# Kernel optimization log

Measured on AMD Instinct MI355X. Metric: run time of the kernel, lower is better.

Reference implementation:

```python
import jax, jax.numpy as jnp
import numpy as np
from jax import lax

EPS = 1e-5
C = 232          # inp == oup
BF = C // 2      # branch_features
GROUPS = 2


def bn(x, g, b, m, v):
    # inference batchnorm over channel axis 1 of NCHW
    scale = g / jnp.sqrt(v + EPS)
    return x * scale[None, :, None, None] + (b - m * scale)[None, :, None, None]


def prelu(x, a):
    return jnp.where(x >= 0, x, a.reshape(()) * x)


def conv1x1(x, w):
    # x: [B,C,H,W], w: [O,C]
    return jnp.einsum('bchw,oc->bohw', x, w)


def dwconv3x3(x, w):
    # depthwise 3x3, stride 1, pad 1; w: [C,1,3,3]
    return lax.conv_general_dilated(
        x, w, window_strides=(1, 1), padding=((1, 1), (1, 1)),
        feature_group_count=x.shape[1],
        dimension_numbers=('NCHW', 'OIHW', 'NCHW'))


def setup_inputs() -> dict:
    key = jax.random.key(0)
    ks = jax.random.split(key, 12)
    B, H, W = 64, 56, 56
    inp = {
        'x': jax.random.normal(ks[0], (B, C, H, W), jnp.float32),
        'w2': jax.random.normal(ks[1], (BF, BF), jnp.float32) * 0.1,
        'bn1_g': jax.random.uniform(ks[2], (BF,), jnp.float32, 0.5, 1.5),
        'bn1_b': jax.random.normal(ks[3], (BF,), jnp.float32) * 0.1,
        'bn1_m': jax.random.normal(ks[4], (BF,), jnp.float32) * 0.1,
        'bn1_v': jax.random.uniform(ks[5], (BF,), jnp.float32, 0.5, 1.5),
        'alpha1': jnp.full((1,), 0.25, jnp.float32),
        'wdw': jax.random.normal(ks[6], (BF, 1, 3, 3), jnp.float32) * 0.1,
        'bn2_g': jax.random.uniform(ks[7], (BF,), jnp.float32, 0.5, 1.5),
        'bn2_b': jax.random.normal(ks[8], (BF,), jnp.float32) * 0.1,
        'bn2_m': jax.random.normal(ks[9], (BF,), jnp.float32) * 0.1,
        'bn2_v': jax.random.uniform(ks[10], (BF,), jnp.float32, 0.5, 1.5),
        'w3': jax.random.normal(ks[11], (BF, BF), jnp.float32) * 0.1,
        'bn3_g': jax.random.uniform(jax.random.fold_in(key, 101), (BF,), jnp.float32, 0.5, 1.5),
        'bn3_b': jax.random.normal(jax.random.fold_in(key, 102), (BF,)) * 0.1,
        'bn3_m': jax.random.normal(jax.random.fold_in(key, 103), (BF,)) * 0.1,
        'bn3_v': jax.random.uniform(jax.random.fold_in(key, 104), (BF,), jnp.float32, 0.5, 1.5),
        'alpha2': jnp.full((1,), 0.25, jnp.float32),
    }
    return inp


def reference(x, w2, bn1_g, bn1_b, bn1_m, bn1_v, alpha1, wdw,
              bn2_g, bn2_b, bn2_m, bn2_v, w3, bn3_g, bn3_b, bn3_m, bn3_v, alpha2):
    # stride == 1 path: split channels in half
    x1, x2 = x[:, :BF], x[:, BF:]
    # branch2: 1x1 conv -> BN -> PReLU -> dw3x3 -> BN -> 1x1 conv -> BN -> PReLU
    h = prelu(bn(conv1x1(x2, w2), bn1_g, bn1_b, bn1_m, bn1_v), alpha1)
    h = bn(dwconv3x3(h, wdw), bn2_g, bn2_b, bn2_m, bn2_v)
    h = prelu(bn(conv1x1(h, w3), bn3_g, bn3_b, bn3_m, bn3_v), alpha2)
    out = jnp.concatenate([x1, h], axis=1)
    # channel shuffle (groups=2): out channel k reads input channel (k%2)*cpg + k//2
    cpg = C // GROUPS
    idx = (jnp.arange(C) % GROUPS) * cpg + jnp.arange(C) // GROUPS
    return out[:, idx]
```

## Files before the change

### kernel.cpp

```cpp
#include <hip/hip_runtime.h>
#include <hip/hip_bf16.h>


#define BATCH 64
#define CTOT  232
#define BFC   116
#define HW    3136
#define WD    56
#define CH2   120
#define EPSV  1e-5f

typedef unsigned short u16;
typedef __attribute__((ext_vector_type(8))) short short8;
typedef __attribute__((ext_vector_type(4))) float float4v;

#define WS_W2P   0
#define WS_W3P   32768
#define WS_WDWT  65536
#define WS_B1P   69888
#define WS_B3P   70400

__device__ __forceinline__ u16 f2bf(float f) {
    union { float f; unsigned u; } v; v.f = f;
    unsigned r = v.u + 0x7FFF + ((v.u >> 16) & 1);
    return (u16)(r >> 16);
}
__device__ __forceinline__ float bf2f(u16 u) {
    union { unsigned u; float f; } v; v.u = ((unsigned)u) << 16;
    return v.f;
}

__global__ __launch_bounds__(256) void prep(
    const float* __restrict__ w2, const float* __restrict__ g1, const float* __restrict__ b1,
    const float* __restrict__ m1, const float* __restrict__ v1,
    const float* __restrict__ wdw,
    const float* __restrict__ g2, const float* __restrict__ b2,
    const float* __restrict__ m2, const float* __restrict__ v2,
    const float* __restrict__ w3, const float* __restrict__ g3, const float* __restrict__ b3,
    const float* __restrict__ m3, const float* __restrict__ v3,
    char* __restrict__ ws) {
    u16* w2p = (u16*)(ws + WS_W2P);
    u16* w3p = (u16*)(ws + WS_W3P);
    float* wdwt = (float*)(ws + WS_WDWT);
    float* b1p = (float*)(ws + WS_B1P);
    float* b3p = (float*)(ws + WS_B3P);
    int tid = threadIdx.x;
    int bx = blockIdx.x;
    if (bx < 8) {
        int o = bx * 16 + (tid >> 4);
        int cs = (tid & 15) * 8;
        float sc = (o < BFC) ? g1[o] * rsqrtf(v1[o] + EPSV) : 0.f;
        short8 v;
        for (int j = 0; j < 8; j++) {
            int c = cs + j;
            float val = (o < BFC && c < BFC) ? sc * w2[o * BFC + c] : 0.f;
            ((u16*)&v)[j] = f2bf(val);
        }
        *(short8*)&w2p[o * 128 + cs] = v;
    } else if (bx < 16) {
        int o = (bx - 8) * 16 + (tid >> 4);
        int cs = (tid & 15) * 8;
        float sc = (o < BFC) ? g3[o] * rsqrtf(v3[o] + EPSV) : 0.f;
        short8 v;
        for (int j = 0; j < 8; j++) {
            int c = cs + j;
            float val = 0.f;
            if (o < BFC && c < BFC) {
                float sc2 = g2[c] * rsqrtf(v2[c] + EPSV);
                val = sc * sc2 * w3[o * BFC + c];
            }
            ((u16*)&v)[j] = f2bf(val);
        }
        *(short8*)&w3p[o * 128 + cs] = v;
    } else {
        if (tid < CH2)
            for (int tap = 0; tap < 9; tap++)
                wdwt[tap * CH2 + tid] = (tid < BFC) ? wdw[tid * 9 + tap] : 0.f;
        if (tid < 128) {
            float b1v = 0.f, b3v = 0.f;
            if (tid < BFC) {
                float sc1 = g1[tid] * rsqrtf(v1[tid] + EPSV);
                b1v = b1[tid] - m1[tid] * sc1;
                float sc3 = g3[tid] * rsqrtf(v3[tid] + EPSV);
                float s = 0.f;
                for (int c = 0; c < BFC; c++) {
                    float sc2 = g2[c] * rsqrtf(v2[c] + EPSV);
                    float sh2 = b2[c] - m2[c] * sc2;
                    s += w3[tid * BFC + c] * sh2;
                }
                b3v = (b3[tid] - m3[tid] * sc3) + sc3 * s;
            }
            b1p[tid] = b1v;
            b3p[tid] = b3v;
        }
    }
}

__device__ __forceinline__ void dw_compute(const u16* xs, const float* __restrict__ wdwt,
                                           int u, short8 hrow[4]) {
    int oct = u % 15;
    int pq = u / 15;
    int rr = pq / 14;
    int col0 = (pq % 14) * 4;
    float acc[4][8];
    #pragma unroll
    for (int i = 0; i < 4; i++)
        #pragma unroll
        for (int j = 0; j < 8; j++) acc[i][j] = 0.f;
    #pragma unroll
    for (int dy = 0; dy < 3; dy++) {
        int lr = rr + dy;
        float f[6][8];
        #pragma unroll
        for (int k = 0; k < 6; k++) {
            int ci = col0 - 1 + k;
            if (ci >= 0 && ci < WD) {
                short8 v = *(const short8*)&xs[(lr * WD + ci) * CH2 + oct * 8];
                #pragma unroll
                for (int j = 0; j < 8; j++) f[k][j] = bf2f(((const u16*)&v)[j]);
            } else {
                #pragma unroll
                for (int j = 0; j < 8; j++) f[k][j] = 0.f;
            }
        }
        #pragma unroll
        for (int dx = 0; dx < 3; dx++) {
            const float* wt = &wdwt[(dy * 3 + dx) * CH2 + oct * 8];
            float4v w0 = *(const float4v*)&wt[0];
            float4v w1 = *(const float4v*)&wt[4];
            float w8[8] = {w0[0], w0[1], w0[2], w0[3], w1[0], w1[1], w1[2], w1[3]};
            #pragma unroll
            for (int i = 0; i < 4; i++)
                #pragma unroll
                for (int j = 0; j < 8; j++)
                    acc[i][j] += f[i + dx][j] * w8[j];
        }
    }
    #pragma unroll
    for (int i = 0; i < 4; i++) {
        short8 ov;
        #pragma unroll
        for (int j = 0; j < 8; j++) ((u16*)&ov)[j] = f2bf(acc[i][j]);
        hrow[i] = ov;
    }
}

__global__ __launch_bounds__(256, 3) void k1(const float* __restrict__ x,
        const float* __restrict__ al1, const float* __restrict__ al2,
        const char* __restrict__ ws, float* __restrict__ out) {
    __shared__ u16 xs[224 * CH2];
    const u16* w2p = (const u16*)(ws + WS_W2P);
    const u16* w3p = (const u16*)(ws + WS_W3P);
    const float* wdwt = (const float*)(ws + WS_WDWT);
    const float* b1p = (const float*)(ws + WS_B1P);
    const float* b3p = (const float*)(ws + WS_B3P);

    int tid = threadIdx.x;
    int lane = tid & 63;
    int w = tid >> 6;
    int l15 = lane & 15, kq = lane >> 4;

    int L = blockIdx.x;
    int sw = (L & 7) * 224 + (L >> 3);
    int b = sw / 28;
    int s = sw - b * 28;
    int r0 = s * 2;
    int p_in0 = r0 * WD - WD;
    int p_out0 = r0 * WD;

    const float* x2 = x + ((size_t)b * CTOT + BFC) * HW;
    float a1 = al1[0];
    float a2 = al2[0];
    short8 z8 = {0, 0, 0, 0, 0, 0, 0, 0};

    #pragma unroll 4
    for (int it = 0; it < 14; it++) {
        int u = it * 256 + tid;
        int c2 = (u >> 3) & 63;
        if (c2 < 60) {
            int q = (u >> 9) * 8 + (u & 7);
            int p = p_in0 + q * 4;
            unsigned pr[4] = {0u, 0u, 0u, 0u};
            if (c2 < 58 && p >= 0 && p < HW) {
                int c = 2 * c2;
                float4v va = *(const float4v*)&x2[(size_t)c * HW + p];
                float4v vb = *(const float4v*)&x2[(size_t)(c + 1) * HW + p];
                #pragma unroll
                for (int j = 0; j < 4; j++)
                    pr[j] = (unsigned)f2bf(va[j]) | ((unsigned)f2bf(vb[j]) << 16);
            }
            int px = q * 4;
            #pragma unroll
            for (int j = 0; j < 4; j++)
                *(unsigned*)&xs[(px + j) * CH2 + 2 * c2] = pr[j];
        }
    }
    __syncthreads();

    {
        short8 bfr[2][4];
        float biasv[2];
        for (int ni = 0; ni < 2; ni++) {
            int o = (2 * w + ni) * 16 + l15;
            #pragma unroll
            for (int kt = 0; kt < 4; kt++)
                bfr[ni][kt] = *(const short8*)&w2p[o * 128 + kt * 32 + kq * 8];
            biasv[ni] = b1p[o];
        }
        for (int mt = 0; mt < 14; mt++) {
            int pl = mt * 16 + l15;
            const u16* arow = &xs[pl * CH2];
            short8 afr[4];
            #pragma unroll
            for (int kt = 0; kt < 4; kt++) {
                short8 av = z8;
                if (!(kt == 3 && kq == 3)) av = *(const short8*)&arow[kt * 32 + kq * 8];
                afr[kt] = av;
            }
            float4v acc[2];
            #pragma unroll
            for (int ni = 0; ni < 2; ni++) {
                acc[ni] = (float4v){0.f, 0.f, 0.f, 0.f};
                #pragma unroll
                for (int kt = 0; kt < 4; kt++)
                    acc[ni] = __builtin_amdgcn_mfma_f32_16x16x32_bf16(afr[kt], bfr[ni][kt], acc[ni], 0, 0, 0);
            }
            __syncthreads();
            #pragma unroll
            for (int ni = 0; ni < 2; ni++) {
                int o = (2 * w + ni) * 16 + l15;
                if (o < CH2) {
                    int plb = mt * 16 + kq * 4;
                    #pragma unroll
                    for (int r = 0; r < 4; r++) {
                        int pl2 = plb + r;
                        int pim = p_in0 + pl2;
                        float y = acc[ni][r] + biasv[ni];
                        y = y >= 0.f ? y : a1 * y;
                        xs[pl2 * CH2 + o] = (pim >= 0 && pim < HW) ? f2bf(y) : (u16)0;
                    }
                }
            }
        }
    }
    __syncthreads();

    short8 hA[4], hB[4];
    int uA = tid, uB = tid + 256;
    bool hasB = uB < 420;
    dw_compute(xs, wdwt, uA, hA);
    if (hasB) dw_compute(xs, wdwt, uB, hB);
    __syncthreads();
    {
        int oct = uA % 15, pq = uA / 15;
        int pl = (pq / 14) * WD + (pq % 14) * 4;
        #pragma unroll
        for (int i = 0; i < 4; i++)
            *(short8*)&xs[(pl + i) * CH2 + oct * 8] = hA[i];
    }
    if (hasB) {
        int oct = uB % 15, pq = uB / 15;
        int pl = (pq / 14) * WD + (pq % 14) * 4;
        #pragma unroll
        for (int i = 0; i < 4; i++)
            *(short8*)&xs[(pl + i) * CH2 + oct * 8] = hB[i];
    }
    __syncthreads();

    {
        int mh = w >> 1, nh = w & 1;
        short8 cfr[4][4];
        float bias3v[4];
        for (int ni = 0; ni < 4; ni++) {
            int o = (nh * 4 + ni) * 16 + l15;
            #pragma unroll
            for (int kt = 0; kt < 4; kt++)
                cfr[ni][kt] = *(const short8*)&w3p[o * 128 + kt * 32 + kq * 8];
            bias3v[ni] = b3p[o];
        }
        #pragma unroll
        for (int mi = 0; mi < 4; mi++) {
            int mt = mh * 4 + mi;
            if (mt < 7) {
                int pl = mt * 16 + l15;
                const u16* arow = &xs[pl * CH2];
                short8 afr[4];
                #pragma unroll
                for (int kt = 0; kt < 4; kt++) {
                    short8 av = z8;
                    if (!(kt == 3 && kq == 3)) av = *(const short8*)&arow[kt * 32 + kq * 8];
                    afr[kt] = av;
                }
                for (int ni = 0; ni < 4; ni++) {
                    float4v acc = {0.f, 0.f, 0.f, 0.f};
                    #pragma unroll
                    for (int kt = 0; kt < 4; kt++)
                        acc = __builtin_amdgcn_mfma_f32_16x16x32_bf16(afr[kt], cfr[ni][kt], acc, 0, 0, 0);
                    int o = (nh * 4 + ni) * 16 + l15;
                    int pq = mt * 16 + kq * 4;
                    if (o < BFC) {
                        float4v ov;
                        #pragma unroll
                        for (int r = 0; r < 4; r++) {
                            float y = acc[r] + bias3v[ni];
                            ov[r] = y >= 0.f ? y : a2 * y;
                        }
                        *(float4v*)&out[((size_t)b * CTOT + 2 * o + 1) * HW + p_out0 + pq] = ov;
                    }
                }
            }
        }
    }

    {
        const float* x1 = x + (size_t)b * CTOT * HW;
        for (int u = tid; u < BFC * 28; u += 256) {
            int c = u / 28, i = u % 28;
            float4v v = *(const float4v*)&x1[(size_t)c * HW + p_out0 + i * 4];
            *(float4v*)&out[((size_t)b * CTOT + 2 * c) * HW + p_out0 + i * 4] = v;
        }
    }
}

extern "C" void kernel_launch(void* const* d_in, const int* in_sizes, int n_in,
                              void* d_out, int out_size, void* d_ws, size_t ws_size,
                              hipStream_t stream) {
    const float* x   = (const float*)d_in[0];
    const float* w2  = (const float*)d_in[1];
    const float* g1  = (const float*)d_in[2];
    const float* b1  = (const float*)d_in[3];
    const float* m1  = (const float*)d_in[4];
    const float* v1  = (const float*)d_in[5];
    const float* al1 = (const float*)d_in[6];
    const float* wdw = (const float*)d_in[7];
    const float* g2  = (const float*)d_in[8];
    const float* b2  = (const float*)d_in[9];
    const float* m2  = (const float*)d_in[10];
    const float* v2  = (const float*)d_in[11];
    const float* w3  = (const float*)d_in[12];
    const float* g3  = (const float*)d_in[13];
    const float* b3  = (const float*)d_in[14];
    const float* m3  = (const float*)d_in[15];
    const float* v3  = (const float*)d_in[16];
    const float* al2 = (const float*)d_in[17];
    float* out = (float*)d_out;
    char* ws = (char*)d_ws;

    hipLaunchKernelGGL(prep, dim3(17), dim3(256), 0, stream,
                       w2, g1, b1, m1, v1, wdw, g2, b2, m2, v2, w3, g3, b3, m3, v3, ws);
    hipLaunchKernelGGL(k1, dim3(28 * BATCH), dim3(256), 0, stream, x, al1, al2, ws, out);
}
```

Before: 575.7 us.

## Partition work by pixel rows per wave to remove block barriers in first GEMM

Each wave now loads and converts its own band of pixel rows and runs the first 1x1 conv over its own M tiles for all output channels. This removes the block-wide barrier after the load and the per-tile barrier inside the first GEMM. The second 1x1 conv is likewise split by M tile per wave over all N, and the x1 passthrough copy moves earlier so its traffic overlaps the depthwise stage. In exchange, weights are reloaded from global or cache per M tile instead of being held in registers, and wave 3 gets less work than the others.

Result: slower. 671.8 us (+16.7%).

```diff
diff --git a/kernel.cpp b/kernel.cpp
--- a/kernel.cpp
+++ b/kernel.cpp
@@ -173,74 +173,89 @@
     float a2 = al2[0];
     short8 z8 = {0, 0, 0, 0, 0, 0, 0, 0};
 
-    #pragma unroll 4
-    for (int it = 0; it < 14; it++) {
-        int u = it * 256 + tid;
-        int c2 = (u >> 3) & 63;
-        if (c2 < 60) {
-            int q = (u >> 9) * 8 + (u & 7);
-            int p = p_in0 + q * 4;
-            unsigned pr[4] = {0u, 0u, 0u, 0u};
-            if (c2 < 58 && p >= 0 && p < HW) {
-                int c = 2 * c2;
-                float4v va = *(const float4v*)&x2[(size_t)c * HW + p];
-                float4v vb = *(const float4v*)&x2[(size_t)(c + 1) * HW + p];
-                #pragma unroll
-                for (int j = 0; j < 4; j++)
-                    pr[j] = (unsigned)f2bf(va[j]) | ((unsigned)f2bf(vb[j]) << 16);
-            }
-            int px = q * 4;
-            #pragma unroll
-            for (int j = 0; j < 4; j++)
-                *(unsigned*)&xs[(px + j) * CH2 + 2 * c2] = pr[j];
-        }
-    }
-    __syncthreads();
+    int mt0 = w * 4;
+    int mtn = (w == 3) ? 2 : 4;
+    int row0 = w * 64;
+    int nrows = (w == 3) ? 32 : 64;
 
     {
-        short8 bfr[2][4];
-        float biasv[2];
-        for (int ni = 0; ni < 2; ni++) {
-            int o = (2 * w + ni) * 16 + l15;
-            #pragma unroll
-            for (int kt = 0; kt < 4; kt++)
-                bfr[ni][kt] = *(const short8*)&w2p[o * 128 + kt * 32 + kq * 8];
-            biasv[ni] = b1p[o];
-        }
-        for (int mt = 0; mt < 14; mt++) {
-            int pl = mt * 16 + l15;
-            const u16* arow = &xs[pl * CH2];
-            short8 afr[4];
-            #pragma unroll
-            for (int kt = 0; kt < 4; kt++) {
-                short8 av = z8;
-                if (!(kt == 3 && kq == 3)) av = *(const short8*)&arow[kt * 32 + kq * 8];
-                afr[kt] = av;
-            }
-            float4v acc[2];
+        int q = lane & 7;
+        int c2l = lane >> 3;
+        for (int rc = 0; rc < nrows; rc += 32) {
+            #pragma unroll
+            for (int c2b = 0; c2b < 64; c2b += 8) {
+                int c2 = c2b + c2l;
+                if (c2 < 60) {
+                    int row = row0 + rc + q * 4;
+                    int p = p_in0 + row;
+                    unsigned pr[4] = {0u, 0u, 0u, 0u};
+                    if (c2 < 58 && p >= 0 && p < HW) {
+                        int c = 2 * c2;
+                        float4v va = *(const float4v*)&x2[(size_t)c * HW + p];
+                        float4v vb = *(const float4v*)&x2[(size_t)(c + 1) * HW + p];
+                        #pragma unroll
+                        for (int j = 0; j < 4; j++)
+                            pr[j] = (unsigned)f2bf(va[j]) | ((unsigned)f2bf(vb[j]) << 16);
+                    }
+                    #pragma unroll
+                    for (int j = 0; j < 4; j++)
+                        *(unsigned*)&xs[(row + j) * CH2 + 2 * c2] = pr[j];
+                }
+            }
+        }
+    }
+
+    for (int mi = 0; mi < mtn; mi++) {
+        int mt = mt0 + mi;
+        int pl = mt * 16 + l15;
+        const u16* arow = &xs[pl * CH2];
+        short8 afr[4];
+        #pragma unroll
+        for (int kt = 0; kt < 4; kt++) {
+            short8 av = z8;
+            if (!(kt == 3 && kq == 3)) av = *(const short8*)&arow[kt * 32 + kq * 8];
+            afr[kt] = av;
+        }
+        #pragma unroll
+        for (int nh = 0; nh < 4; nh++) {
+            short8 bfr[2][4];
+            float biasv[2];
             #pragma unroll
             for (int ni = 0; ni < 2; ni++) {
-                acc[ni] = (float4v){0.f, 0.f, 0.f, 0.f};
+                int o = nh * 32 + ni * 16 + l15;
                 #pragma unroll
                 for (int kt = 0; kt < 4; kt++)
-                    acc[ni] = __builtin_amdgcn_mfma_f32_16x16x32_bf16(afr[kt], bfr[ni][kt], acc[ni], 0, 0, 0);
-            }
-            __syncthreads();
+                    bfr[ni][kt] = *(const short8*)&w2p[o * 128 + kt * 32 + kq * 8];
+                biasv[ni] = b1p[o];
+            }
             #pragma unroll
             for (int ni = 0; ni < 2; ni++) {
-                int o = (2 * w + ni) * 16 + l15;
+                float4v acc = {0.f, 0.f, 0.f, 0.f};
+                #pragma unroll
+                for (int kt = 0; kt < 4; kt++)
+                    acc = __builtin_amdgcn_mfma_f32_16x16x32_bf16(afr[kt], bfr[ni][kt], acc, 0, 0, 0);
+                int o = nh * 32 + ni * 16 + l15;
                 if (o < CH2) {
                     int plb = mt * 16 + kq * 4;
                     #pragma unroll
                     for (int r = 0; r < 4; r++) {
                         int pl2 = plb + r;
                         int pim = p_in0 + pl2;
-                        float y = acc[ni][r] + biasv[ni];
+                        float y = acc[r] + biasv[ni];
                         y = y >= 0.f ? y : a1 * y;
                         xs[pl2 * CH2 + o] = (pim >= 0 && pim < HW) ? f2bf(y) : (u16)0;
                     }
                 }
             }
+        }
+    }
+
+    {
+        const float* x1 = x + (size_t)b * CTOT * HW;
+        for (int u = tid; u < BFC * 28; u += 256) {
+            int c = u / 28, i = u % 28;
+            float4v v = *(const float4v*)&x1[(size_t)c * HW + p_out0 + i * 4];
+            *(float4v*)&out[((size_t)b * CTOT + 2 * c) * HW + p_out0 + i * 4] = v;
         }
     }
     __syncthreads();
@@ -268,35 +283,38 @@
     __syncthreads();
 
     {
-        int mh = w >> 1, nh = w & 1;
-        short8 cfr[4][4];
-        float bias3v[4];
-        for (int ni = 0; ni < 4; ni++) {
-            int o = (nh * 4 + ni) * 16 + l15;
-            #pragma unroll
-            for (int kt = 0; kt < 4; kt++)
-                cfr[ni][kt] = *(const short8*)&w3p[o * 128 + kt * 32 + kq * 8];
-            bias3v[ni] = b3p[o];
-        }
-        #pragma unroll
-        for (int mi = 0; mi < 4; mi++) {
-            int mt = mh * 4 + mi;
-            if (mt < 7) {
-                int pl = mt * 16 + l15;
-                const u16* arow = &xs[pl * CH2];
-                short8 afr[4];
-                #pragma unroll
-                for (int kt = 0; kt < 4; kt++) {
-                    short8 av = z8;
-                    if (!(kt == 3 && kq == 3)) av = *(const short8*)&arow[kt * 32 + kq * 8];
-                    afr[kt] = av;
-                }
-                for (int ni = 0; ni < 4; ni++) {
+        int ct0 = w * 2;
+        int ctn = (w == 3) ? 1 : 2;
+        for (int mi = 0; mi < ctn; mi++) {
+            int mt = ct0 + mi;
+            int pl = mt * 16 + l15;
+            const u16* arow = &xs[pl * CH2];
+            short8 afr[4];
+            #pragma unroll
+            for (int kt = 0; kt < 4; kt++) {
+                short8 av = z8;
+                if (!(kt == 3 && kq == 3)) av = *(const short8*)&arow[kt * 32 + kq * 8];
+                afr[kt] = av;
+            }
+            #pragma unroll
+            for (int nh = 0; nh < 4; nh++) {
+                short8 cfr[2][4];
+                float bias3v[2];
+                #pragma unroll
+                for (int ni = 0; ni < 2; ni++) {
+                    int o = nh * 32 + ni * 16 + l15;
+                    #pragma unroll
+                    for (int kt = 0; kt < 4; kt++)
+                        cfr[ni][kt] = *(const short8*)&w3p[o * 128 + kt * 32 + kq * 8];
+                    bias3v[ni] = b3p[o];
+                }
+                #pragma unroll
+                for (int ni = 0; ni < 2; ni++) {
                     float4v acc = {0.f, 0.f, 0.f, 0.f};
                     #pragma unroll
                     for (int kt = 0; kt < 4; kt++)
                         acc = __builtin_amdgcn_mfma_f32_16x16x32_bf16(afr[kt], cfr[ni][kt], acc, 0, 0, 0);
-                    int o = (nh * 4 + ni) * 16 + l15;
+                    int o = nh * 32 + ni * 16 + l15;
                     int pq = mt * 16 + kq * 4;
                     if (o < BFC) {
                         float4v ov;
@@ -309,15 +327,6 @@
                     }
                 }
             }
-        }
-    }
-
-    {
-        const float* x1 = x + (size_t)b * CTOT * HW;
-        for (int u = tid; u < BFC * 28; u += 256) {
-            int c = u / 28, i = u % 28;
-            float4v v = *(const float4v*)&x1[(size_t)c * HW + p_out0 + i * 4];
-            *(float4v*)&out[((size_t)b * CTOT + 2 * c) * HW + p_out0 + i * 4] = v;
         }
     }
 }
```
